# Kernel tuning notes

Measured on AMD Instinct MI355X. Metric: run time of the kernel, lower is better.

## Reference

```python
import jax, jax.numpy as jnp
import numpy as np

THETA = 10000.0

def _rope(t):
    # lucidrains-style interleaved rotary over the FULL last dim (dim=hidden_size)
    T, d = t.shape[-2], t.shape[-1]
    freqs = 1.0 / (THETA ** (jnp.arange(0, d, 2, dtype=jnp.float32) / d))  # (d/2,)
    ang = jnp.arange(T, dtype=jnp.float32)[:, None] * freqs[None, :]       # (T, d/2)
    ang = jnp.repeat(ang, 2, axis=-1)                                      # (T, d) interleaved
    cos, sin = jnp.cos(ang), jnp.sin(ang)
    x = t.reshape(t.shape[:-1] + (d // 2, 2))
    x1, x2 = x[..., 0], x[..., 1]
    rot = jnp.stack([-x2, x1], axis=-1).reshape(t.shape)  # rotate_half, interleaved pairs
    return t * cos + rot * sin


def setup_inputs() -> dict:
    key = jax.random.key(0)
    ks = jax.random.split(key, 5)
    B, T, C = 4, 2048, 1024
    s = 0.02
    return {
        "x":  jax.random.normal(ks[0], (B, T, C), dtype=jnp.float32),
        "Wq": jax.random.normal(ks[1], (C, C), dtype=jnp.float32) * s,
        "bq": jnp.zeros((C,), dtype=jnp.float32),
        "Wk": jax.random.normal(ks[2], (C, C), dtype=jnp.float32) * s,
        "bk": jnp.zeros((C,), dtype=jnp.float32),
        "Wv": jax.random.normal(ks[3], (C, C), dtype=jnp.float32) * s,
        "bv": jnp.zeros((C,), dtype=jnp.float32),
        "Wf": jax.random.normal(ks[4], (C, C), dtype=jnp.float32) * s,
        "bf": jnp.zeros((C,), dtype=jnp.float32),
    }


def reference(x, Wq, bq, Wk, bk, Wv, bv, Wf, bf):
    B, T, C = x.shape
    Q = _rope(x @ Wq.T + bq)
    K = _rope(x @ Wk.T + bk)
    V = x @ Wv.T + bv
    # scores [B,T,T]; _get_D(gamma=1, T) is exactly a causal lower-triangular mask
    A = jnp.einsum('btd,bsd->bts', Q, K) / jnp.sqrt(jnp.float32(C))
    causal = jnp.tril(jnp.ones((T, T), dtype=bool))
    A = jnp.where(causal, A, -jnp.inf)
    A = jax.nn.softmax(A, axis=-1)
    out = jnp.einsum('bts,bsd->btd', A, V)
    return out @ Wf.T + bf
```

## Files before the change

### kernel.cpp

```cpp
#include <hip/hip_runtime.h>
#include <math.h>


#define AS1(p) ((__attribute__((address_space(1))) void*)(p))
#define AS3(p) ((__attribute__((address_space(3))) void*)(p))

typedef __attribute__((ext_vector_type(8))) short bf16x8;
typedef __attribute__((ext_vector_type(4))) float f32x4;

__device__ __forceinline__ unsigned short f2bf(float f) {
  unsigned int u = __float_as_uint(f);
  u += 0x7fffu + ((u >> 16) & 1u);
  return (unsigned short)(u >> 16);
}

__global__ __launch_bounds__(256) void cast_all(
    const float* __restrict__ x, const float* __restrict__ Wq,
    const float* __restrict__ Wk, const float* __restrict__ Wv,
    const float* __restrict__ Wf,
    unsigned short* __restrict__ xb, unsigned short* __restrict__ Wqb,
    unsigned short* __restrict__ Wkb, unsigned short* __restrict__ Wvb,
    unsigned short* __restrict__ Wfb, float* __restrict__ rsum) {
  int i = blockIdx.x * 256 + threadIdx.x;
  if (i < 8192) rsum[i] = 0.0f;
  const float* src; unsigned short* dst; int off;
  if (i < 2097152) { src = x; dst = xb; off = i; }
  else {
    int j = i - 2097152;
    int w = j >> 18; off = j & 262143;
    src = (w == 0) ? Wq : (w == 1) ? Wk : (w == 2) ? Wv : Wf;
    dst = (w == 0) ? Wqb : (w == 1) ? Wkb : (w == 2) ? Wvb : Wfb;
  }
  float4 f = ((const float4*)src)[off];
  ushort4 o;
  o.x = f2bf(f.x); o.y = f2bf(f.y); o.z = f2bf(f.z); o.w = f2bf(f.w);
  ((ushort4*)dst)[off] = o;
}

__device__ __forceinline__ void repack_store_mi(unsigned short (&vals)[4][4],
                                                unsigned short* sh, int mi,
                                                int m0, int n0, long long ldo,
                                                unsigned short* __restrict__ Out) {
  const int tid = threadIdx.x, lane = tid & 63, w = tid >> 6;
  const int half = w & 1, wn = (w >> 1) << 6;
  const int cl = lane & 15, q4 = lane >> 4;
  const int lr = half * 16 + q4 * 4;
#pragma unroll
  for (int ni = 0; ni < 4; ni++)
#pragma unroll
    for (int rr = 0; rr < 4; rr++)
      sh[(lr + rr) * 132 + wn + ni * 16 + cl] = vals[ni][rr];
  __syncthreads();
#pragma unroll
  for (int it = 0; it < 2; ++it) {
    int row = (tid >> 4) + it * 16;
    int c8 = (tid & 15) << 3;
    bf16x8 v = *(const bf16x8*)(sh + row * 132 + c8);
    int gr = m0 + (row < 16 ? mi * 16 + row : 48 + mi * 16 + row);
    *(bf16x8*)(Out + (long long)gr * ldo + n0 + c8) = v;
  }
  __syncthreads();
}

__device__ __forceinline__ void core4(
    const unsigned short* __restrict__ A, long long lda,
    const unsigned short* __restrict__ B, long long ldb,
    int nkt, f32x4 (&acc)[4][4], unsigned short* lds) {
  const int tid  = threadIdx.x;
  const int lane = tid & 63;
  const int w    = tid >> 6;
  const int wr   = w >> 2;
  const int wc   = w & 3;
  const int fr   = lane & 15;
  const int fq   = lane >> 4;
  const int csel = (fq ^ ((fr >> 1) & 3)) << 3;
  const int srow = tid >> 2;
  const int scsw = ((tid & 3) ^ ((srow >> 1) & 3)) << 3;
  const unsigned short* Asrc  = A + (long long)srow * lda + scsw;
  const unsigned short* Bsrc0 = B + (long long)srow * ldb + scsw;
  const unsigned short* Bsrc1 = B + (long long)(srow + 128) * ldb + scsw;
  unsigned short* dsta = lds + tid * 8;

  auto stage = [&](int kt) {
    const int bo = (kt & 3) * 12288;
    const long long ko = (long long)kt * 32;
    __builtin_amdgcn_global_load_lds(AS1(Asrc + ko),  AS3(dsta + bo),        16, 0, 0);
    __builtin_amdgcn_global_load_lds(AS1(Bsrc0 + ko), AS3(dsta + bo + 4096), 16, 0, 0);
    __builtin_amdgcn_global_load_lds(AS1(Bsrc1 + ko), AS3(dsta + bo + 8192), 16, 0, 0);
  };
  auto rdfrag = [&](int kt, bf16x8 (&r)[8]) {
    const unsigned short* Ab = lds + (kt & 3) * 12288 + (wr * 64 + fr) * 32 + csel;
    const unsigned short* Bb = lds + (kt & 3) * 12288 + 4096 + (wc * 64 + fr) * 32 + csel;
#pragma unroll
    for (int mi = 0; mi < 4; ++mi) r[mi] = *(const bf16x8*)(Ab + mi * 512);
#pragma unroll
    for (int nj = 0; nj < 4; ++nj) r[4 + nj] = *(const bf16x8*)(Bb + nj * 512);
  };

  bf16x8 ra[8], rb[8];
  stage(0); stage(1); stage(2);
  asm volatile("s_waitcnt vmcnt(6)" ::: "memory");
  __builtin_amdgcn_s_barrier();
  rdfrag(0, ra);

  auto body = [&](int kt, bf16x8 (&cur)[8], bf16x8 (&nxt)[8]) {
    if (kt + 3 < nkt) {
      stage(kt + 3);
      asm volatile("s_waitcnt vmcnt(6)" ::: "memory");
    } else if (kt + 2 < nkt) {
      asm volatile("s_waitcnt vmcnt(3)" ::: "memory");
    } else if (kt + 1 < nkt) {
      asm volatile("s_waitcnt vmcnt(0)" ::: "memory");
    }
    if (kt + 1 < nkt) {
      __builtin_amdgcn_s_barrier();
      rdfrag(kt + 1, nxt);
    }
    __builtin_amdgcn_s_setprio(1);
#pragma unroll
    for (int mi = 0; mi < 4; ++mi)
#pragma unroll
      for (int nj = 0; nj < 4; ++nj)
        acc[mi][nj] = __builtin_amdgcn_mfma_f32_16x16x32_bf16(cur[mi], cur[4 + nj], acc[mi][nj], 0, 0, 0);
    __builtin_amdgcn_s_setprio(0);
    if (kt + 1 < nkt) __builtin_amdgcn_s_barrier();
  };

#pragma unroll 1
  for (int kt = 0; kt < nkt; kt += 2) {
    body(kt, ra, rb);
    body(kt + 1, rb, ra);
  }
}

__device__ __forceinline__ void core4h(
    const unsigned short* __restrict__ A, long long lda,
    const unsigned short* __restrict__ B, long long ldb,
    int nkt, f32x4 (&acc)[4][4], unsigned short* lds) {
  const int tid  = threadIdx.x;
  const int lane = tid & 63;
  const int w    = tid >> 6;
  const int wm   = (w & 1) << 6;
  const int wn   = (w >> 1) << 6;
  const int fr   = lane & 15;
  const int fq   = lane >> 4;
  const int csel = (fq ^ ((fr >> 1) & 3)) << 3;
  const int srow = tid >> 2;
  const int scsw = ((tid & 3) ^ ((srow >> 1) & 3)) << 3;
  const unsigned short* Asrc0 = A + (long long)srow * lda + scsw;
  const unsigned short* Asrc1 = A + (long long)(srow + 64) * lda + scsw;
  const unsigned short* Bsrc0 = B + (long long)srow * ldb + scsw;
  const unsigned short* Bsrc1 = B + (long long)(srow + 64) * ldb + scsw;
  unsigned short* dsta = lds + tid * 8;

  auto stage = [&](int kt) {
    const int bo = (kt % 3) * 8192;
    const long long ko = (long long)kt * 32;
    __builtin_amdgcn_global_load_lds(AS1(Asrc0 + ko), AS3(dsta + bo),        16, 0, 0);
    __builtin_amdgcn_global_load_lds(AS1(Asrc1 + ko), AS3(dsta + bo + 2048), 16, 0, 0);
    __builtin_amdgcn_global_load_lds(AS1(Bsrc0 + ko), AS3(dsta + bo + 4096), 16, 0, 0);
    __builtin_amdgcn_global_load_lds(AS1(Bsrc1 + ko), AS3(dsta + bo + 6144), 16, 0, 0);
  };
  auto rdfrag = [&](int kt, bf16x8 (&r)[8]) {
    const unsigned short* Ab = lds + (kt % 3) * 8192 + (wm + fr) * 32 + csel;
    const unsigned short* Bb = lds + (kt % 3) * 8192 + 4096 + (wn + fr) * 32 + csel;
#pragma unroll
    for (int mi = 0; mi < 4; ++mi) r[mi] = *(const bf16x8*)(Ab + mi * 512);
#pragma unroll
    for (int nj = 0; nj < 4; ++nj) r[4 + nj] = *(const bf16x8*)(Bb + nj * 512);
  };

  bf16x8 ra[8], rb[8];
  stage(0); stage(1);
  asm volatile("s_waitcnt vmcnt(4)" ::: "memory");
  __builtin_amdgcn_s_barrier();
  rdfrag(0, ra);

  auto body = [&](int kt, bf16x8 (&cur)[8], bf16x8 (&nxt)[8]) {
    if (kt + 2 < nkt) {
      stage(kt + 2);
      asm volatile("s_waitcnt vmcnt(4)" ::: "memory");
    } else if (kt + 1 < nkt) {
      asm volatile("s_waitcnt vmcnt(0)" ::: "memory");
    }
    if (kt + 1 < nkt) {
      __builtin_amdgcn_s_barrier();
      rdfrag(kt + 1, nxt);
    }
    __builtin_amdgcn_s_setprio(1);
#pragma unroll
    for (int mi = 0; mi < 4; ++mi)
#pragma unroll
      for (int nj = 0; nj < 4; ++nj)
        acc[mi][nj] = __builtin_amdgcn_mfma_f32_16x16x32_bf16(cur[mi], cur[4 + nj], acc[mi][nj], 0, 0, 0);
    __builtin_amdgcn_s_setprio(0);
    if (kt + 1 < nkt) __builtin_amdgcn_s_barrier();
  };

#pragma unroll 1
  for (int kt = 0; kt < nkt; kt += 2) {
    body(kt, ra, rb);
    body(kt + 1, rb, ra);
  }
}

__global__ __launch_bounds__(512, 2) void proj_rope(
    const unsigned short* __restrict__ xb,
    const unsigned short* __restrict__ Wq, const unsigned short* __restrict__ Wk,
    const unsigned short* __restrict__ Wv,
    const float* __restrict__ bq, const float* __restrict__ bk, const float* __restrict__ bv,
    unsigned short* __restrict__ Q, unsigned short* __restrict__ Ko,
    unsigned short* __restrict__ Vt, const int which) {
  __shared__ unsigned short lds[49152];
  const int tid = threadIdx.x, lane = tid & 63, w = tid >> 6;
  const int wr = w >> 2, wc = w & 3;
  const int cl = lane & 15, q4 = lane >> 4;

  f32x4 acc[4][4];
#pragma unroll
  for (int i = 0; i < 4; i++)
#pragma unroll
    for (int j = 0; j < 4; j++)
#pragma unroll
      for (int k = 0; k < 4; k++) acc[i][j][k] = 0.0f;

  if (which == 2) {
    const int p = blockIdx.x + 64 * blockIdx.y;
    const int m0 = ((p >> 3) & 7) * 128;
    const int n0 = (4 * (p & 7) + (p >> 6)) * 256;
    core4(Wv + (long long)m0 * 1024, 1024, xb + (long long)n0 * 1024, 1024, 32, acc, lds);
    __syncthreads();
    const int b = n0 >> 11, sloc = n0 & 2047;
#pragma unroll
    for (int mi = 0; mi < 4; ++mi) {
      const int lr = wr * 64 + mi * 16 + q4 * 4;
#pragma unroll
      for (int rr = 0; rr < 4; ++rr) {
        const float b_ = bv[m0 + lr + rr];
#pragma unroll
        for (int nj = 0; nj < 4; ++nj)
          lds[(lr + rr) * 264 + wc * 64 + nj * 16 + cl] = f2bf(acc[mi][nj][rr] + b_);
      }
    }
    __syncthreads();
    unsigned short* Outb = Vt + (long long)b * 1024 * 2048;
#pragma unroll
    for (int it = 0; it < 8; ++it) {
      int c = it * 512 + tid;
      int row = c >> 5, c8 = (c & 31) << 3;
      bf16x8 v = *(const bf16x8*)(lds + row * 264 + c8);
      *(bf16x8*)(Outb + (long long)(m0 + row) * 2048 + sloc + c8) = v;
    }
    return;
  }

  const int m0 = blockIdx.x * 128;
  const int n0 = blockIdx.y * 256;
  const unsigned short* W = which == 0 ? Wq : Wk;
  const float* bias = which == 0 ? bq : bk;
  unsigned short* Out = which == 0 ? Q : Ko;

  core4(xb + (long long)m0 * 1024, 1024, W + (long long)n0 * 1024, 1024, 32, acc, lds);
  __syncthreads();

  const float NEG_L2T_512 = -0.025952563239354392f;
  const float INV2PI = 0.15915494309189535f;
  float freqn[4];
#pragma unroll
  for (int nj = 0; nj < 4; ++nj) {
    int gn = n0 + wc * 64 + nj * 16 + cl;
    freqn[nj] = exp2f(NEG_L2T_512 * (float)(gn >> 1));
  }
#pragma unroll
  for (int mi = 0; mi < 4; ++mi) {
    const int lr = wr * 64 + mi * 16 + q4 * 4;
    const int t0 = (m0 & 2047) + lr;
#pragma unroll
    for (int nj = 0; nj < 4; ++nj) {
      const int gn = n0 + wc * 64 + nj * 16 + cl;
      const float bi = bias[gn];
#pragma unroll
      for (int rr = 0; rr < 4; ++rr) {
        float v = acc[mi][nj][rr] + bi;
        float partner = __shfl_xor(v, 1, 64);
        float ang = (float)(t0 + rr) * freqn[nj];
        float rev = ang * INV2PI;
        rev = rev - floorf(rev);
        float c_ = __builtin_amdgcn_cosf(rev);
        float s_ = __builtin_amdgcn_sinf(rev);
        v = v * c_ + ((gn & 1) ? partner : -partner) * s_;
        lds[(lr + rr) * 264 + wc * 64 + nj * 16 + cl] = f2bf(v);
      }
    }
  }
  __syncthreads();
#pragma unroll
  for (int it = 0; it < 8; ++it) {
    int c = it * 512 + tid;
    int row = c >> 5, c8 = (c & 31) << 3;
    bf16x8 v = *(const bf16x8*)(lds + row * 264 + c8);
    *(bf16x8*)(Out + (long long)(m0 + row) * 1024 + n0 + c8) = v;
  }
}

__global__ __launch_bounds__(256, 2) void score_exp(const unsigned short* __restrict__ Q,
                                                    const unsigned short* __restrict__ Kk,
                                                    unsigned short* __restrict__ P,
                                                    float* __restrict__ row_sum) {
  __shared__ unsigned short sh[24576];
  const int flat = blockIdx.x;
  const int swz = (flat & 7) * 68 + (flat >> 3);
  const int b = swz / 136;
  const int bx = swz % 136;
  int i = (int)((sqrtf(8.0f * (float)bx + 1.0f) - 1.0f) * 0.5f);
  while ((i + 1) * (i + 2) / 2 <= bx) ++i;
  while (i * (i + 1) / 2 > bx) --i;
  const int j = bx - i * (i + 1) / 2;
  const int m0 = i * 128, n0 = j * 128;
  const unsigned short* Qb = Q + (long long)b * 2048 * 1024;
  const unsigned short* Kb = Kk + (long long)b * 2048 * 1024;
  unsigned short* Pb = P + (long long)b * 2048 * 2048;
  float* rs = row_sum + b * 2048;

  f32x4 acc[4][4];
#pragma unroll
  for (int ii = 0; ii < 4; ii++)
#pragma unroll
    for (int jj = 0; jj < 4; jj++)
#pragma unroll
      for (int k = 0; k < 4; k++) acc[ii][jj][k] = 0.0f;

  core4h(Qb + (long long)m0 * 1024, 1024, Kb + (long long)n0 * 1024, 1024, 32, acc, sh);
  __syncthreads();

  const int tid = threadIdx.x, lane = tid & 63, w = tid >> 6;
  const int wm = (w & 1) << 6, wn = (w >> 1) << 6;
  const int cl = lane & 15, q4 = lane >> 4;
  const bool diag = (i == j);
#pragma unroll
  for (int mi = 0; mi < 4; mi++) {
    unsigned short vals[4][4];
    float rsum[4] = {0.f, 0.f, 0.f, 0.f};
#pragma unroll
    for (int ni = 0; ni < 4; ni++) {
      const int gn = n0 + wn + ni * 16 + cl;
#pragma unroll
      for (int rr = 0; rr < 4; rr++) {
        const int gm = m0 + wm + mi * 16 + q4 * 4 + rr;
        float e = (diag && gn > gm) ? 0.0f : __expf(acc[mi][ni][rr] * 0.03125f);
        vals[ni][rr] = f2bf(e);
        rsum[rr] += e;
      }
    }
#pragma unroll
    for (int rr = 0; rr < 4; rr++) {
#pragma unroll
      for (int off = 1; off < 16; off <<= 1) rsum[rr] += __shfl_xor(rsum[rr], off, 64);
    }
    if (cl == 0) {
      const int gm = m0 + wm + mi * 16 + q4 * 4;
#pragma unroll
      for (int rr = 0; rr < 4; rr++) atomicAdd(&rs[gm + rr], rsum[rr]);
    }
    repack_store_mi(vals, sh, mi, m0, n0, 2048, Pb);
  }
}

__global__ __launch_bounds__(256, 2) void pv_gemm(const unsigned short* __restrict__ P,
                                                  const unsigned short* __restrict__ Vt,
                                                  const float* __restrict__ row_sum,
                                                  unsigned short* __restrict__ O) {
  __shared__ unsigned short sh[24576];
  const int p = blockIdx.x;
  const int xcd = p & 7;
  const int idx = p >> 3;
  const int g = idx >> 3;
  const int dt = idx & 7;
  const int b  = (g < 4) ? g : g - 4;
  const int mt = (g < 4) ? 15 - xcd : xcd;
  const int m0 = mt * 128;
  const int n0 = dt * 128;
  const unsigned short* Pb = P + (long long)b * 2048 * 2048;
  const unsigned short* Vb = Vt + (long long)b * 1024 * 2048;
  const float* rs = row_sum + b * 2048;
  const int nkt = 4 * (mt + 1);

  f32x4 acc[4][4];
#pragma unroll
  for (int i = 0; i < 4; i++)
#pragma unroll
    for (int j = 0; j < 4; j++)
#pragma unroll
      for (int k = 0; k < 4; k++) acc[i][j][k] = 0.0f;

  core4h(Pb + (long long)m0 * 2048, 2048, Vb + (long long)n0 * 2048, 2048, nkt, acc, sh);
  __syncthreads();

  const int tid = threadIdx.x, lane = tid & 63, w = tid >> 6;
  const int wm = (w & 1) << 6;
  const int q4 = lane >> 4;
#pragma unroll
  for (int mi = 0; mi < 4; mi++) {
    unsigned short vals[4][4];
    float inv[4];
    const int gm0 = m0 + wm + mi * 16 + q4 * 4;
#pragma unroll
    for (int rr = 0; rr < 4; rr++) inv[rr] = 1.0f / rs[gm0 + rr];
#pragma unroll
    for (int ni = 0; ni < 4; ni++)
#pragma unroll
      for (int rr = 0; rr < 4; rr++)
        vals[ni][rr] = f2bf(acc[mi][ni][rr] * inv[rr]);
    repack_store_mi(vals, sh, mi, m0, n0, 1024, O + (long long)b * 2048 * 1024);
  }
}

__global__ __launch_bounds__(512, 2) void final_gemm(const unsigned short* __restrict__ O,
                                                     const unsigned short* __restrict__ Wf,
                                                     const float* __restrict__ bf_,
                                                     float* __restrict__ out) {
  __shared__ unsigned short lds[49152];
  float* shf = (float*)lds;
  const int tid = threadIdx.x, lane = tid & 63, w = tid >> 6;
  const int wr = w >> 2, wc = w & 3;
  const int cl = lane & 15, q4 = lane >> 4;
  const int m0 = blockIdx.x * 128;
  const int n0 = blockIdx.y * 256;

  f32x4 acc[4][4];
#pragma unroll
  for (int i = 0; i < 4; i++)
#pragma unroll
    for (int j = 0; j < 4; j++)
#pragma unroll
      for (int k = 0; k < 4; k++) acc[i][j][k] = 0.0f;

  core4(O + (long long)m0 * 1024, 1024, Wf + (long long)n0 * 1024, 1024, 32, acc, lds);

#pragma unroll
  for (int r = 0; r < 2; ++r) {
    __syncthreads();
    if (wr == r) {
#pragma unroll
      for (int mi = 0; mi < 4; ++mi)
#pragma unroll
        for (int nj = 0; nj < 4; ++nj) {
          const int col = wc * 64 + nj * 16 + cl;
          const float bi = bf_[n0 + col];
#pragma unroll
          for (int rr = 0; rr < 4; ++rr)
            shf[(mi * 16 + q4 * 4 + rr) * 260 + col] = acc[mi][nj][rr] + bi;
        }
    }
    __syncthreads();
#pragma unroll
    for (int it = 0; it < 8; ++it) {
      int c = it * 512 + tid;
      int row = c >> 6, c4 = (c & 63) << 2;
      float4 v = *(const float4*)(shf + row * 260 + c4);
      *(float4*)(out + (long long)(m0 + r * 64 + row) * 1024 + n0 + c4) = v;
    }
  }
}

extern "C" void kernel_launch(void* const* d_in, const int* in_sizes, int n_in,
                              void* d_out, int out_size, void* d_ws, size_t ws_size,
                              hipStream_t stream) {
  (void)in_sizes; (void)n_in; (void)out_size; (void)ws_size;
  const float* x   = (const float*)d_in[0];
  const float* Wq  = (const float*)d_in[1];
  const float* bq  = (const float*)d_in[2];
  const float* Wk  = (const float*)d_in[3];
  const float* bk  = (const float*)d_in[4];
  const float* Wv  = (const float*)d_in[5];
  const float* bv  = (const float*)d_in[6];
  const float* Wf  = (const float*)d_in[7];
  const float* bf_ = (const float*)d_in[8];
  float* out = (float*)d_out;

  char* ws = (char*)d_ws;
  const size_t MB = 1024 * 1024;
  unsigned short* xb  = (unsigned short*)(ws);
  unsigned short* Wqb = (unsigned short*)(ws + 16 * MB);
  unsigned short* Wkb = (unsigned short*)(ws + 18 * MB);
  unsigned short* Wvb = (unsigned short*)(ws + 20 * MB);
  unsigned short* Wfb = (unsigned short*)(ws + 22 * MB);
  unsigned short* Qb  = (unsigned short*)(ws + 24 * MB);
  unsigned short* Kb  = (unsigned short*)(ws + 40 * MB);
  unsigned short* Vtb = (unsigned short*)(ws + 56 * MB);
  unsigned short* Ob  = (unsigned short*)(ws + 72 * MB);
  unsigned short* Pb  = (unsigned short*)(ws + 88 * MB);
  float*          rsum= (float*)(ws + 120 * MB);

  cast_all<<<dim3(3145728 / 256), dim3(256), 0, stream>>>(x, Wq, Wk, Wv, Wf, xb, Wqb, Wkb, Wvb, Wfb, rsum);
  proj_rope<<<dim3(64, 4), dim3(512), 0, stream>>>(xb, Wqb, Wkb, Wvb, bq, bk, bv, Qb, Kb, Vtb, 0);
  proj_rope<<<dim3(64, 4), dim3(512), 0, stream>>>(xb, Wqb, Wkb, Wvb, bq, bk, bv, Qb, Kb, Vtb, 1);
  proj_rope<<<dim3(64, 4), dim3(512), 0, stream>>>(xb, Wqb, Wkb, Wvb, bq, bk, bv, Qb, Kb, Vtb, 2);
  score_exp<<<dim3(544), dim3(256), 0, stream>>>(Qb, Kb, Pb, rsum);
  pv_gemm<<<dim3(512), dim3(256), 0, stream>>>(Pb, Vtb, rsum, Ob);
  final_gemm<<<dim3(64, 4), dim3(512), 0, stream>>>(Ob, Wfb, bf_, out);
}
```

Before: 271.0 us.

## Merge Q/K/V projection launches into one swizzled 128x128-tile kernel

Replaces three 256-block proj_rope launches (512 threads, 128x256 tiles) with a single 1536-block launch of 256-thread blocks on 128x128 tiles. The flat block index is swizzled across XCDs and selects Q, K or V. The epilogue now writes through a per-mi repack helper into smaller shared memory instead of a full-tile LDS staging pass. This is meant to cut launch gaps and tail effects and to fill more CUs concurrently. In exchange, weight and input reuse per tile drops and the helpers core4h and repack_store_mi must exist elsewhere.

```diff
diff --git a/kernel.cpp b/kernel.cpp
--- a/kernel.cpp
+++ b/kernel.cpp
@@ -204,16 +204,20 @@
   }
 }
 
-__global__ __launch_bounds__(512, 2) void proj_rope(
+__global__ __launch_bounds__(256, 2) void proj_rope(
     const unsigned short* __restrict__ xb,
     const unsigned short* __restrict__ Wq, const unsigned short* __restrict__ Wk,
     const unsigned short* __restrict__ Wv,
     const float* __restrict__ bq, const float* __restrict__ bk, const float* __restrict__ bv,
     unsigned short* __restrict__ Q, unsigned short* __restrict__ Ko,
-    unsigned short* __restrict__ Vt, const int which) {
-  __shared__ unsigned short lds[49152];
+    unsigned short* __restrict__ Vt) {
+  __shared__ unsigned short sh[24576];
+  const int flat = blockIdx.x;
+  const int swz = (flat & 7) * 192 + (flat >> 3);
+  const int which = swz >> 9;
+  const int t = swz & 511;
   const int tid = threadIdx.x, lane = tid & 63, w = tid >> 6;
-  const int wr = w >> 2, wc = w & 3;
+  const int wm = (w & 1) << 6, wn = (w >> 1) << 6;
   const int cl = lane & 15, q4 = lane >> 4;
 
   f32x4 acc[4][4];
@@ -225,81 +229,66 @@
       for (int k = 0; k < 4; k++) acc[i][j][k] = 0.0f;
 
   if (which == 2) {
-    const int p = blockIdx.x + 64 * blockIdx.y;
-    const int m0 = ((p >> 3) & 7) * 128;
-    const int n0 = (4 * (p & 7) + (p >> 6)) * 256;
-    core4(Wv + (long long)m0 * 1024, 1024, xb + (long long)n0 * 1024, 1024, 32, acc, lds);
+    const int d0 = (t & 7) * 128;
+    const int s0 = (t >> 3) * 128;
+    core4h(Wv + (long long)d0 * 1024, 1024, xb + (long long)s0 * 1024, 1024, 32, acc, sh);
     __syncthreads();
-    const int b = n0 >> 11, sloc = n0 & 2047;
-#pragma unroll
-    for (int mi = 0; mi < 4; ++mi) {
-      const int lr = wr * 64 + mi * 16 + q4 * 4;
-#pragma unroll
-      for (int rr = 0; rr < 4; ++rr) {
-        const float b_ = bv[m0 + lr + rr];
-#pragma unroll
-        for (int nj = 0; nj < 4; ++nj)
-          lds[(lr + rr) * 264 + wc * 64 + nj * 16 + cl] = f2bf(acc[mi][nj][rr] + b_);
+    const int b = s0 >> 11, sloc = s0 & 2047;
+    unsigned short* Outb = Vt + (long long)b * 1024 * 2048;
+#pragma unroll
+    for (int mi = 0; mi < 4; mi++) {
+      unsigned short vals[4][4];
+#pragma unroll
+      for (int rr = 0; rr < 4; rr++) {
+        const float b_ = bv[d0 + wm + mi * 16 + q4 * 4 + rr];
+#pragma unroll
+        for (int ni = 0; ni < 4; ni++)
+          vals[ni][rr] = f2bf(acc[mi][ni][rr] + b_);
       }
-    }
-    __syncthreads();
-    unsigned short* Outb = Vt + (long long)b * 1024 * 2048;
-#pragma unroll
-    for (int it = 0; it < 8; ++it) {
-      int c = it * 512 + tid;
-      int row = c >> 5, c8 = (c & 31) << 3;
-      bf16x8 v = *(const bf16x8*)(lds + row * 264 + c8);
-      *(bf16x8*)(Outb + (long long)(m0 + row) * 2048 + sloc + c8) = v;
+      repack_store_mi(vals, sh, mi, d0, sloc, 2048, Outb);
     }
     return;
   }
 
-  const int m0 = blockIdx.x * 128;
-  const int n0 = blockIdx.y * 256;
+  const int m0 = (t >> 3) * 128;
+  const int n0 = (t & 7) * 128;
   const unsigned short* W = which == 0 ? Wq : Wk;
   const float* bias = which == 0 ? bq : bk;
   unsigned short* Out = which == 0 ? Q : Ko;
 
-  core4(xb + (long long)m0 * 1024, 1024, W + (long long)n0 * 1024, 1024, 32, acc, lds);
+  core4h(xb + (long long)m0 * 1024, 1024, W + (long long)n0 * 1024, 1024, 32, acc, sh);
   __syncthreads();
 
   const float NEG_L2T_512 = -0.025952563239354392f;
   const float INV2PI = 0.15915494309189535f;
   float freqn[4];
 #pragma unroll
-  for (int nj = 0; nj < 4; ++nj) {
-    int gn = n0 + wc * 64 + nj * 16 + cl;
-    freqn[nj] = exp2f(NEG_L2T_512 * (float)(gn >> 1));
-  }
-#pragma unroll
-  for (int mi = 0; mi < 4; ++mi) {
-    const int lr = wr * 64 + mi * 16 + q4 * 4;
-    const int t0 = (m0 & 2047) + lr;
-#pragma unroll
-    for (int nj = 0; nj < 4; ++nj) {
-      const int gn = n0 + wc * 64 + nj * 16 + cl;
+  for (int ni = 0; ni < 4; ni++) {
+    int gn = n0 + wn + ni * 16 + cl;
+    freqn[ni] = exp2f(NEG_L2T_512 * (float)(gn >> 1));
+  }
+#pragma unroll
+  for (int mi = 0; mi < 4; mi++) {
+    unsigned short vals[4][4];
+    const int t0 = (m0 & 2047) + wm + mi * 16 + q4 * 4;
+#pragma unroll
+    for (int ni = 0; ni < 4; ni++) {
+      const int gn = n0 + wn + ni * 16 + cl;
       const float bi = bias[gn];
 #pragma unroll
-      for (int rr = 0; rr < 4; ++rr) {
-        float v = acc[mi][nj][rr] + bi;
+      for (int rr = 0; rr < 4; rr++) {
+        float v = acc[mi][ni][rr] + bi;
         float partner = __shfl_xor(v, 1, 64);
-        float ang = (float)(t0 + rr) * freqn[nj];
+        float ang = (float)(t0 + rr) * freqn[ni];
         float rev = ang * INV2PI;
         rev = rev - floorf(rev);
         float c_ = __builtin_amdgcn_cosf(rev);
         float s_ = __builtin_amdgcn_sinf(rev);
         v = v * c_ + ((gn & 1) ? partner : -partner) * s_;
-        lds[(lr + rr) * 264 + wc * 64 + nj * 16 + cl] = f2bf(v);
+        vals[ni][rr] = f2bf(v);
       }
     }
-  }
-  __syncthreads();
-#pragma unroll
-  for (int it = 0; it < 8; ++it) {
-    int c = it * 512 + tid;
-    int row = c >> 5, c8 = (c & 31) << 3;
-    bf16x8 v = *(const bf16x8*)(lds + row * 264 + c8);
-    *(bf16x8*)(Out + (long long)(m0 + row) * 1024 + n0 + c8) = v;
+    repack_store_mi(vals, sh, mi, m0, n0, 1024, Out);
   }
 }
 
@@ -493,9 +482,7 @@
   float*          rsum= (float*)(ws + 120 * MB);
 
   cast_all<<<dim3(3145728 / 256), dim3(256), 0, stream>>>(x, Wq, Wk, Wv, Wf, xb, Wqb, Wkb, Wvb, Wfb, rsum);
-  proj_rope<<<dim3(64, 4), dim3(512), 0, stream>>>(xb, Wqb, Wkb, Wvb, bq, bk, bv, Qb, Kb, Vtb, 0);
-  proj_rope<<<dim3(64, 4), dim3(512), 0, stream>>>(xb, Wqb, Wkb, Wvb, bq, bk, bv, Qb, Kb, Vtb, 1);
-  proj_rope<<<dim3(64, 4), dim3(512), 0, stream>>>(xb, Wqb, Wkb, Wvb, bq, bk, bv, Qb, Kb, Vtb, 2);
+  proj_rope<<<dim3(1536), dim3(256), 0, stream>>>(xb, Wqb, Wkb, Wvb, bq, bk, bv, Qb, Kb, Vtb);
   score_exp<<<dim3(544), dim3(256), 0, stream>>>(Qb, Kb, Pb, rsum);
   pv_gemm<<<dim3(512), dim3(256), 0, stream>>>(Pb, Vtb, rsum, Ob);
   final_gemm<<<dim3(64, 4), dim3(512), 0, stream>>>(Ob, Wfb, bf_, out);
```

New measurement: 275.8 us. About the same (+1.8%).
